# Performance work log

Hardware: AMD Instinct MI355X
Metric: run time of the kernel (lower is better)

Reference implementation:

```python
import jax, jax.numpy as jnp
import numpy as np

H = 64          # hidden_size
NG = 5000       # num_genes
B = 32          # num_graphs
N = B * NG      # total nodes
E = 1_600_000   # total edges


def setup_inputs() -> dict:
    key = jax.random.key(0)
    ks = jax.random.split(key, 32)
    def nrm(k, shape, s=0.05):
        return jax.random.normal(k, shape, jnp.float32) * s
    return {
        "x": jax.random.normal(ks[0], (N, 2), jnp.float32),
        "edge_index": jax.random.randint(ks[1], (2, E), 0, N),
        # pert_w: Linear(1, H); gene_basal_w: Linear(1, H)
        "pert_w_W": nrm(ks[2], (H, 1)), "pert_w_b": nrm(ks[3], (H,)),
        "basal_W": nrm(ks[4], (H, 1)), "basal_b": nrm(ks[5], (H,)),
        # gene embedding table (max_norm=True -> rows renormed to norm<=1)
        "emb_table": nrm(ks[6], (NG, H), 0.5),
        # emb_trans: Linear(2H, H)
        "emb_trans_W": nrm(ks[7], (H, 2 * H)), "emb_trans_b": nrm(ks[8], (H,)),
        # pert_base_trans_w: Linear(2H, H)  (gene_pert_agg == 'concat+w')
        "pbt_W": nrm(ks[9], (H, 2 * H)), "pbt_b": nrm(ks[10], (H,)),
        # two GCNConv(H, H) layers
        "gcn1_W": nrm(ks[11], (H, H)), "gcn1_b": nrm(ks[12], (H,)),
        "gcn2_W": nrm(ks[13], (H, H)), "gcn2_b": nrm(ks[14], (H,)),
        # recovery_w: MLP([H, 2H, H, 1]) with BN on first two hidden layers
        "rec_W1": nrm(ks[15], (2 * H, H)), "rec_b1": nrm(ks[16], (2 * H,)),
        "rec_g1": jnp.ones((2 * H,), jnp.float32), "rec_be1": jnp.zeros((2 * H,), jnp.float32),
        "rec_W2": nrm(ks[17], (H, 2 * H)), "rec_b2": nrm(ks[18], (H,)),
        "rec_g2": jnp.ones((H,), jnp.float32), "rec_be2": jnp.zeros((H,), jnp.float32),
        "rec_W3": nrm(ks[19], (1, H)), "rec_b3": nrm(ks[20], (1,)),
    }


def _gcn_conv(h, src, dst, norm, W, b, n_nodes):
    # PyG GCNConv: x' = scatter_add(norm * (x W^T)[src] -> dst) + b, self-loops included in src/dst
    m = h @ W.T                                   # [N, H]
    out = jax.ops.segment_sum(m[src] * norm[:, None], dst, num_segments=n_nodes)
    return out + b


def _batchnorm(z, g, b, eps=1e-5):
    mu = z.mean(0)
    var = z.var(0)
    return (z - mu) * jax.lax.rsqrt(var + eps) * g + b


def reference(x, edge_index, pert_w_W, pert_w_b, basal_W, basal_b, emb_table,
              emb_trans_W, emb_trans_b, pbt_W, pbt_b, gcn1_W, gcn1_b,
              gcn2_W, gcn2_b, rec_W1, rec_b1, rec_g1, rec_be1,
              rec_W2, rec_b2, rec_g2, rec_be2, rec_W3, rec_b3):
    n_nodes = x.shape[0]
    ng = emb_table.shape[0]
    nb = n_nodes // ng

    # GCN normalization with self-loops (computed once, shared by both layers)
    loop = jnp.arange(n_nodes)
    src = jnp.concatenate([edge_index[0], loop])
    dst = jnp.concatenate([edge_index[1], loop])
    deg = jax.ops.segment_sum(jnp.ones_like(src, jnp.float32), dst, num_segments=n_nodes)
    dinv = jnp.where(deg > 0, jax.lax.rsqrt(jnp.maximum(deg, 1.0)), 0.0)
    norm = dinv[src] * dinv[dst]

    pert_emb = x[:, 1:2] @ pert_w_W.T + pert_w_b          # [N, H]
    base = x[:, 0:1] @ basal_W.T + basal_b                # [N, H]

    # nn.Embedding(max_norm=True): renorm rows to max L2 norm of 1
    nrm = jnp.linalg.norm(emb_table, axis=1, keepdims=True)
    emb_n = emb_table * jnp.minimum(1.0, 1.0 / jnp.maximum(nrm, 1e-7))
    emb = jnp.tile(emb_n, (nb, 1))                        # arange(NG).repeat(B) lookup
    base_emb = jnp.concatenate([emb, base], axis=1) @ emb_trans_W.T + emb_trans_b

    def pbt(p, b_):
        return jnp.concatenate([p, b_], axis=1) @ pbt_W.T + pbt_b

    h = pbt(pert_emb, base_emb)
    h = pbt(jax.nn.relu(_gcn_conv(h, src, dst, norm, gcn1_W, gcn1_b, n_nodes)), base_emb)
    h = pbt(jax.nn.relu(_gcn_conv(h, src, dst, norm, gcn2_W, gcn2_b, n_nodes)), base_emb)

    # recovery_w: Linear -> BN -> ReLU -> Linear -> BN -> ReLU -> Linear
    z = jax.nn.relu(_batchnorm(h @ rec_W1.T + rec_b1, rec_g1, rec_be1))
    z = jax.nn.relu(_batchnorm(z @ rec_W2.T + rec_b2, rec_g2, rec_be2))
    out = z @ rec_W3.T + rec_b3                           # [N, 1]
    return out.reshape(nb, ng)
```

## Files before the change

### kernel.cpp

```cpp
#include <hip/hip_runtime.h>


#define GS_GRID 2048
#define GS_BLK  256

enum { A1_=0, A0_=64, C1_=128, C0_=192, D1_=256, D0_=320,
       S1_=384, Q1_=512, SC1_=640, SH1_=768,
       S2_=896, Q2_=960, SC2_=1024, SH2_=1088,
       GD1_=1152, GA1_=1216, G00_=1280, CST_FLOATS=2048 };

__device__ __forceinline__ float wave_sum64(float v) {
#pragma unroll
  for (int o = 32; o; o >>= 1) v += __shfl_xor(v, o, 64);
  return v;
}

__device__ __forceinline__ int rfl(int v) { return __builtin_amdgcn_readfirstlane(v); }

__device__ __forceinline__ float rlane(float v, int k) {
  return __int_as_float(__builtin_amdgcn_readlane(__float_as_int(v), k));
}


__global__ __launch_bounds__(256) void hist_k(const int* __restrict__ ei,
                                              int* __restrict__ hist, int E) {
  __shared__ int h[256];
  const int t = threadIdx.x;
  h[t] = 0;
  __syncthreads();
  const int per = (E + gridDim.x - 1) / gridDim.x;
  const int beg = blockIdx.x * per, end = min(E, beg + per);
  for (int i = beg + t; i < end; i += 256)
    atomicAdd(&h[ei[E + i] >> 10], 1);
  __syncthreads();
  hist[blockIdx.x * 256 + t] = h[t];
}

__global__ void bscan_k(int* __restrict__ hist, int* __restrict__ bucketBase,
                        int* __restrict__ rowptrN, int E, int nblk) {
  const int t = threadIdx.x;
  int run = 0;
  for (int b = 0; b < nblk; ++b) {
    int v = hist[b * 256 + t];
    hist[b * 256 + t] = run;
    run += v;
  }
  __shared__ int sc[256];
  sc[t] = run; __syncthreads();
  for (int o = 1; o < 256; o <<= 1) {
    int x = sc[t]; if (t >= o) x += sc[t - o];
    __syncthreads(); sc[t] = x; __syncthreads();
  }
  bucketBase[t] = sc[t] - run;
  if (t == 255) { bucketBase[256] = sc[t]; rowptrN[0] = E; }
}

__global__ __launch_bounds__(256) void bucket_k(const int* __restrict__ ei,
                                                const int* __restrict__ hist,
                                                const int* __restrict__ bucketBase,
                                                int2* __restrict__ eb, int E) {
  __shared__ int cur[256];
  const int t = threadIdx.x;
  cur[t] = hist[blockIdx.x * 256 + t] + bucketBase[t];
  __syncthreads();
  const int per = (E + gridDim.x - 1) / gridDim.x;
  const int beg = blockIdx.x * per, end = min(E, beg + per);
  for (int i = beg + t; i < end; i += 256) {
    int s = ei[i], d = ei[E + i];
    int pos = atomicAdd(&cur[d >> 10], 1);
    eb[pos] = make_int2(s, d);
  }
}

__global__ __launch_bounds__(256) void csr_k(const int2* __restrict__ eb,
                                             const int* __restrict__ bucketBase,
                                             int* __restrict__ rowptr, float* __restrict__ dinv,
                                             int* __restrict__ col, int N) {
  __shared__ int cnt[1024];
  __shared__ int base[1024];
  __shared__ int red[256];
  const int t = threadIdx.x;
  const int k = blockIdx.x;
  const int nodeBeg = k << 10;
  const int segBeg = bucketBase[k], segEnd = bucketBase[k + 1];
#pragma unroll
  for (int j = t; j < 1024; j += 256) cnt[j] = 0;
  __syncthreads();
  for (int i = segBeg + t; i < segEnd; i += 256)
    atomicAdd(&cnt[eb[i].y & 1023], 1);
  __syncthreads();
  int c0 = cnt[4 * t], c1 = cnt[4 * t + 1], c2 = cnt[4 * t + 2], c3 = cnt[4 * t + 3];
  int ts = c0 + c1 + c2 + c3;
  red[t] = ts; __syncthreads();
  for (int o = 1; o < 256; o <<= 1) {
    int x = red[t]; if (t >= o) x += red[t - o];
    __syncthreads(); red[t] = x; __syncthreads();
  }
  int off = red[t] - ts;
  base[4 * t] = off;
  base[4 * t + 1] = off + c0;
  base[4 * t + 2] = off + c0 + c1;
  base[4 * t + 3] = off + c0 + c1 + c2;
#pragma unroll
  for (int u = 0; u < 4; ++u) {
    int j = 4 * t + u;
    int node = nodeBeg + j;
    if (node < N) {
      rowptr[node] = segBeg + base[j];
      dinv[node] = rsqrtf((float)(cnt[j] + 1));
    }
  }
  __syncthreads();
  cnt[4 * t] = base[4 * t]; cnt[4 * t + 1] = base[4 * t + 1];
  cnt[4 * t + 2] = base[4 * t + 2]; cnt[4 * t + 3] = base[4 * t + 3];
  __syncthreads();
  for (int i = segBeg + t; i < segEnd; i += 256) {
    int2 e = eb[i];
    int pos = atomicAdd(&cnt[e.y & 1023], 1);
    col[segBeg + pos] = e.x;
  }
}

__global__ void consts1_k(const float* __restrict__ pbtW, const float* __restrict__ pertW,
                          const float* __restrict__ pertB, const float* __restrict__ etW,
                          const float* __restrict__ basW, const float* __restrict__ basB,
                          const float* __restrict__ etB, float* __restrict__ cst) {
  int h = threadIdx.x;
  float a1 = 0, a0 = 0, c1 = 0, c0 = 0;
  for (int k = 0; k < 64; ++k) {
    float wp = pbtW[h * 128 + k];
    a1 = fmaf(wp, pertW[k], a1);
    a0 = fmaf(wp, pertB[k], a0);
    float we = etW[h * 128 + 64 + k];
    c1 = fmaf(we, basW[k], c1);
    c0 = fmaf(we, basB[k], c0);
  }
  cst[A1_ + h] = a1; cst[A0_ + h] = a0; cst[C1_ + h] = c1; cst[C0_ + h] = c0 + etB[h];
}

__global__ void consts2_k(const float* __restrict__ pbtW, const float* __restrict__ pbtB,
                          float* __restrict__ cst) {
  int h = threadIdx.x;
  float d1 = 0, d0 = 0;
  for (int k = 0; k < 64; ++k) {
    float w = pbtW[h * 128 + 64 + k];
    d1 = fmaf(w, cst[C1_ + k], d1);
    d0 = fmaf(w, cst[C0_ + k], d0);
  }
  cst[D1_ + h] = d1; cst[D0_ + h] = d0 + pbtB[h];
}

__global__ void consts3_k(const float* __restrict__ g1W, float* __restrict__ cst) {
  int h = threadIdx.x;
  float gd1 = 0, ga1 = 0, g00 = 0;
  for (int k = 0; k < 64; ++k) {
    float w = g1W[h * 64 + k];
    gd1 = fmaf(w, cst[D1_ + k], gd1);
    ga1 = fmaf(w, cst[A1_ + k], ga1);
    g00 = fmaf(w, cst[D0_ + k] + cst[A0_ + k], g00);
  }
  cst[GD1_ + h] = gd1; cst[GA1_ + h] = ga1; cst[G00_ + h] = g00;
}

template <bool NORM>
__global__ __launch_bounds__(256) void geneT_k(const float* __restrict__ in,
                                               const float* __restrict__ W, int ldw,
                                               float* __restrict__ out, int NG) {
  const int lane = threadIdx.x & 63;
  const int wid = blockIdx.x * 4 + (threadIdx.x >> 6);
  const int nw = gridDim.x * 4;
  float w[64];
#pragma unroll
  for (int j = 0; j < 16; ++j) {
    float4 v = *reinterpret_cast<const float4*>(W + lane * ldw + 4 * j);
    w[4 * j] = v.x; w[4 * j + 1] = v.y; w[4 * j + 2] = v.z; w[4 * j + 3] = v.w;
  }
  for (int g = wid; g < NG; g += nw) {
    float e = in[g * 64 + lane];
    if (NORM) {
      float sq = wave_sum64(e * e);
      float nrm = sqrtf(sq);
      float s = nrm > 1.f ? 1.f / nrm : 1.f;
      e *= s;
    }
    float acc = 0.f;
#pragma unroll
    for (int k = 0; k < 64; ++k) acc = fmaf(w[k], rlane(e, k), acc);
    out[g * 64 + lane] = acc;
  }
}

__global__ __launch_bounds__(256) void h0m1_k(const float* __restrict__ x,
                                              const float* __restrict__ embT2,
                                              const float* __restrict__ embTm1,
                                              const float* __restrict__ dinv,
                                              const float* __restrict__ cst,
                                              float* __restrict__ pb2, float* __restrict__ m1,
                                              int N, int NG) {
  int total = N * 16;
  for (int idx = blockIdx.x * blockDim.x + threadIdx.x; idx < total;
       idx += gridDim.x * blockDim.x) {
    int n = idx >> 4, q = idx & 15;
    int g = n % NG;
    float x0 = x[2 * n], x1 = x[2 * n + 1], dn = dinv[n];
    float4 e2 = *reinterpret_cast<const float4*>(embT2 + g * 64 + q * 4);
    float4 em = *reinterpret_cast<const float4*>(embTm1 + g * 64 + q * 4);
    float4 d1 = *reinterpret_cast<const float4*>(cst + D1_ + q * 4);
    float4 d0 = *reinterpret_cast<const float4*>(cst + D0_ + q * 4);
    float4 gd1 = *reinterpret_cast<const float4*>(cst + GD1_ + q * 4);
    float4 ga1 = *reinterpret_cast<const float4*>(cst + GA1_ + q * 4);
    float4 g00 = *reinterpret_cast<const float4*>(cst + G00_ + q * 4);
    float4 pv, mv;
    pv.x = fmaf(x0, d1.x, e2.x + d0.x); pv.y = fmaf(x0, d1.y, e2.y + d0.y);
    pv.z = fmaf(x0, d1.z, e2.z + d0.z); pv.w = fmaf(x0, d1.w, e2.w + d0.w);
    mv.x = dn * (fmaf(x0, gd1.x, fmaf(x1, ga1.x, em.x + g00.x)));
    mv.y = dn * (fmaf(x0, gd1.y, fmaf(x1, ga1.y, em.y + g00.y)));
    mv.z = dn * (fmaf(x0, gd1.z, fmaf(x1, ga1.z, em.z + g00.z)));
    mv.w = dn * (fmaf(x0, gd1.w, fmaf(x1, ga1.w, em.w + g00.w)));
    reinterpret_cast<float4*>(pb2)[idx] = pv;
    reinterpret_cast<float4*>(m1)[idx] = mv;
  }
}

#define XS_STRIDE 130
#define WS_STRIDE 68
#define OS_STRIDE 68
#define OS_WORDS  (128 * OS_STRIDE)
#define WS_WORDS  (64 * WS_STRIDE)
#define LDS_WORDS (OS_WORDS + WS_WORDS + 128)

template <int LDIN, bool BN, bool MUL_D, bool STATS>
__global__ __launch_bounds__(256, 4) void gemmt_k(const float* __restrict__ in, int inOff,
                                                  const float* __restrict__ W, int ldw,
                                                  const float* __restrict__ bias,
                                                  const float* __restrict__ bnsc,
                                                  const float* __restrict__ bnsh,
                                                  const float* __restrict__ addv,
                                                  const float* __restrict__ dinv,
                                                  float* __restrict__ out, int ldout,
                                                  float* __restrict__ sums,
                                                  float* __restrict__ sqs, int N) {
  __shared__ float lds[LDS_WORDS];
  float* Xs = lds;
  float* Ws = lds + OS_WORDS;
  float* sred = lds + OS_WORDS + WS_WORDS;
  const int t = threadIdx.x;
  const int base = blockIdx.x << 7;
  if (STATS && t < 128) sred[t] = 0.f;

#pragma unroll
  for (int c = 0; c < 16; ++c) {
    int lin = c * 256 + t;
    int cw = lin >> 6, kw = lin & 63;
    Ws[kw * WS_STRIDE + cw] = W[cw * ldw + kw];
  }
#pragma unroll
  for (int c = 0; c < 8; ++c) {
    int lin = c * 256 + t;
    int nl = lin >> 4, k4 = lin & 15;
    int row = base + nl; if (row >= N) row = N - 1;
    float4 v = *reinterpret_cast<const float4*>(in + (size_t)row * LDIN + inOff + 4 * k4);
    if (BN) {
      float4 sc = *reinterpret_cast<const float4*>(bnsc + 4 * k4);
      float4 sh = *reinterpret_cast<const float4*>(bnsh + 4 * k4);
      v.x = fmaxf(fmaf(v.x, sc.x, sh.x), 0.f);
      v.y = fmaxf(fmaf(v.y, sc.y, sh.y), 0.f);
      v.z = fmaxf(fmaf(v.z, sc.z, sh.z), 0.f);
      v.w = fmaxf(fmaf(v.w, sc.w, sh.w), 0.f);
    }
    Xs[(4 * k4 + 0) * XS_STRIDE + nl] = v.x;
    Xs[(4 * k4 + 1) * XS_STRIDE + nl] = v.y;
    Xs[(4 * k4 + 2) * XS_STRIDE + nl] = v.z;
    Xs[(4 * k4 + 3) * XS_STRIDE + nl] = v.w;
  }
  __syncthreads();

  const int ng = t & 31;
  const int c0 = (t >> 5) * 8;
  float acc[8][4];
#pragma unroll
  for (int i = 0; i < 8; ++i)
#pragma unroll
    for (int j = 0; j < 4; ++j) acc[i][j] = 0.f;
#pragma unroll 4
  for (int k = 0; k < 64; ++k) {
    float4 wa = *reinterpret_cast<const float4*>(Ws + k * WS_STRIDE + c0);
    float4 wb = *reinterpret_cast<const float4*>(Ws + k * WS_STRIDE + c0 + 4);
    float2 xa = *reinterpret_cast<const float2*>(Xs + k * XS_STRIDE + 2 * ng);
    float2 xb = *reinterpret_cast<const float2*>(Xs + k * XS_STRIDE + 2 * ng + 64);
    const float w8[8] = {wa.x, wa.y, wa.z, wa.w, wb.x, wb.y, wb.z, wb.w};
    const float x4[4] = {xa.x, xa.y, xb.x, xb.y};
#pragma unroll
    for (int ci = 0; ci < 8; ++ci)
#pragma unroll
      for (int xi = 0; xi < 4; ++xi)
        acc[ci][xi] = fmaf(w8[ci], x4[xi], acc[ci][xi]);
  }
  __syncthreads();

  const int nd[4] = {2 * ng, 2 * ng + 1, 2 * ng + 64, 2 * ng + 65};
#pragma unroll
  for (int ci = 0; ci < 8; ++ci) {
    Xs[nd[0] * OS_STRIDE + c0 + ci] = acc[ci][0];
    Xs[nd[1] * OS_STRIDE + c0 + ci] = acc[ci][1];
    Xs[nd[2] * OS_STRIDE + c0 + ci] = acc[ci][2];
    Xs[nd[3] * OS_STRIDE + c0 + ci] = acc[ci][3];
  }
  __syncthreads();

  const int q = t & 15;
  float4 bb = make_float4(0.f, 0.f, 0.f, 0.f);
  if (bias) bb = *reinterpret_cast<const float4*>(bias + 4 * q);
  float4 s4 = make_float4(0.f, 0.f, 0.f, 0.f);
  float4 q4 = make_float4(0.f, 0.f, 0.f, 0.f);
#pragma unroll
  for (int c = 0; c < 8; ++c) {
    int nl = c * 16 + (t >> 4);
    int n = base + nl;
    if (n < N) {
      float4 o = *reinterpret_cast<const float4*>(Xs + nl * OS_STRIDE + 4 * q);
      if (MUL_D) {
        float dv = dinv[n];
        o.x *= dv; o.y *= dv; o.z *= dv; o.w *= dv;
      }
      o.x += bb.x; o.y += bb.y; o.z += bb.z; o.w += bb.w;
      if (addv) {
        float4 av = *reinterpret_cast<const float4*>(addv + (size_t)n * 64 + 4 * q);
        o.x += av.x; o.y += av.y; o.z += av.z; o.w += av.w;
      }
      *reinterpret_cast<float4*>(out + (size_t)n * ldout + 4 * q) = o;
      if (STATS) {
        s4.x += o.x; s4.y += o.y; s4.z += o.z; s4.w += o.w;
        q4.x += o.x * o.x; q4.y += o.y * o.y; q4.z += o.z * o.z; q4.w += o.w * o.w;
      }
    }
  }
  if (STATS) {
    atomicAdd(&sred[4 * q + 0], s4.x);
    atomicAdd(&sred[4 * q + 1], s4.y);
    atomicAdd(&sred[4 * q + 2], s4.z);
    atomicAdd(&sred[4 * q + 3], s4.w);
    atomicAdd(&sred[64 + 4 * q + 0], q4.x);
    atomicAdd(&sred[64 + 4 * q + 1], q4.y);
    atomicAdd(&sred[64 + 4 * q + 2], q4.z);
    atomicAdd(&sred[64 + 4 * q + 3], q4.w);
    __syncthreads();
    if (t < 64) {
      atomicAdd(&sums[t], sred[t]);
      atomicAdd(&sqs[t], sred[64 + t]);
    }
  }
}

__global__ __launch_bounds__(256) void gather_k(const float* __restrict__ m,
                                                const int* __restrict__ rowptr,
                                                const int* __restrict__ col,
                                                const float* __restrict__ dinv,
                                                const float* __restrict__ bias,
                                                float* __restrict__ out, int N) {
  const int lane = threadIdx.x & 63;
  const int wid = blockIdx.x * 4 + (threadIdx.x >> 6);
  const int nw = gridDim.x * 4;
  const float b = bias[lane];
  for (int n = wid; n < N; n += nw) {
    const int nn = rfl(n);
    const float dn = dinv[nn];
    float acc = m[(size_t)nn * 64 + lane];
    float acc2 = 0.f;
    const int beg = rfl(rowptr[nn]), end = rfl(rowptr[nn + 1]);
    for (int base = beg; base < end; base += 64) {
      const int rem = end - base;
      const int kk = rem < 64 ? rem : 64;
      int cv = (lane < kk) ? col[base + lane] : 0;
      int k = 0;
      for (; k + 3 < kk; k += 4) {
        int i0 = __shfl(cv, k, 64), i1 = __shfl(cv, k + 1, 64);
        int i2 = __shfl(cv, k + 2, 64), i3 = __shfl(cv, k + 3, 64);
        float v0 = m[(size_t)i0 * 64 + lane];
        float v1 = m[(size_t)i1 * 64 + lane];
        float v2 = m[(size_t)i2 * 64 + lane];
        float v3 = m[(size_t)i3 * 64 + lane];
        acc += v0 + v2; acc2 += v1 + v3;
      }
      for (; k < kk; ++k) acc += m[(size_t)__shfl(cv, k, 64) * 64 + lane];
    }
    out[(size_t)nn * 64 + lane] = fmaxf(fmaf(dn, acc + acc2, b), 0.f);
  }
}

__global__ void bnparam_k(const float* __restrict__ sums, const float* __restrict__ sqs,
                          const float* __restrict__ g, const float* __restrict__ be,
                          float* __restrict__ scale, float* __restrict__ shift, int C,
                          float invN) {
  int t = threadIdx.x;
  if (t < C) {
    float mu = sums[t] * invN;
    float var = fmaxf(sqs[t] * invN - mu * mu, 0.f);
    float sc = g[t] * rsqrtf(var + 1e-5f);
    scale[t] = sc;
    shift[t] = be[t] - mu * sc;
  }
}

__global__ __launch_bounds__(256) void rec3_k(const float* __restrict__ z2,
                                              const float* __restrict__ scale,
                                              const float* __restrict__ shift,
                                              const float* __restrict__ W3,
                                              const float* __restrict__ b3,
                                              float* __restrict__ out, int N) {
  const int lane = threadIdx.x & 63;
  const int wid = blockIdx.x * 4 + (threadIdx.x >> 6);
  const int nw = gridDim.x * 4;
  const float sc = scale[lane], sh = shift[lane], w = W3[lane], b = b3[0];
  for (int n = wid; n < N; n += nw) {
    float v = z2[(size_t)n * 64 + lane];
    v = fmaxf(fmaf(v, sc, sh), 0.f) * w;
    v = wave_sum64(v);
    if (lane == 0) out[n] = v + b;
  }
}

extern "C" void kernel_launch(void* const* d_in, const int* in_sizes, int n_in,
                              void* d_out, int out_size, void* d_ws, size_t ws_size,
                              hipStream_t stream) {
  const float* x     = (const float*)d_in[0];
  const int*   ei    = (const int*)d_in[1];
  const float* pertW = (const float*)d_in[2];
  const float* pertB = (const float*)d_in[3];
  const float* basW  = (const float*)d_in[4];
  const float* basB  = (const float*)d_in[5];
  const float* embTb = (const float*)d_in[6];
  const float* etW   = (const float*)d_in[7];
  const float* etB   = (const float*)d_in[8];
  const float* pbtW  = (const float*)d_in[9];
  const float* pbtB  = (const float*)d_in[10];
  const float* g1W   = (const float*)d_in[11];
  const float* g1B   = (const float*)d_in[12];
  const float* g2W   = (const float*)d_in[13];
  const float* g2B   = (const float*)d_in[14];
  const float* rW1   = (const float*)d_in[15];
  const float* rb1   = (const float*)d_in[16];
  const float* rg1   = (const float*)d_in[17];
  const float* rbe1  = (const float*)d_in[18];
  const float* rW2   = (const float*)d_in[19];
  const float* rb2   = (const float*)d_in[20];
  const float* rg2   = (const float*)d_in[21];
  const float* rbe2  = (const float*)d_in[22];
  const float* rW3   = (const float*)d_in[23];
  const float* rb3   = (const float*)d_in[24];
  float* outp = (float*)d_out;

  const int N  = in_sizes[0] / 2;
  const int E  = in_sizes[1] / 2;
  const int NG = in_sizes[6] / 64;
  const int NB = (N + 1023) >> 10;
  const int NT = (N + 127) >> 7;

  char* p = (char*)d_ws;
  float* cst   = (float*)p; p += CST_FLOATS * 4;
  int*   hist  = (int*)p;   p += 256 * 256 * 4;
  int*   bb    = (int*)p;   p += 1024;
  int*   rowptr= (int*)p;   p += (size_t)(N + 64) * 4;
  float* dinv  = (float*)p; p += (size_t)N * 4;
  int*   col   = (int*)p;   p += (size_t)E * 4;
  float* embT  = (float*)p; p += (size_t)NG * 64 * 4;
  float* embT2 = (float*)p; p += (size_t)NG * 64 * 4;
  float* pb2   = (float*)p; p += (size_t)N * 64 * 4;
  float* hb    = (float*)p; p += (size_t)N * 64 * 4;
  float* tmp1  = (float*)p; p += (size_t)N * 64 * 4;
  float* tmp2  = (float*)p; p += (size_t)N * 64 * 4;
  float* Z   = tmp1;
  float* z2  = pb2;
  float* prt = hb;
  float* embTm1 = embT;
  int2*  eb = (int2*)tmp2;

  dim3 blk(GS_BLK), grid(GS_GRID);

  hipMemsetAsync(cst, 0, CST_FLOATS * 4, stream);

  hist_k<<<256, 256, 0, stream>>>(ei, hist, E);
  bscan_k<<<1, 256, 0, stream>>>(hist, bb, rowptr + N, E, 256);
  bucket_k<<<256, 256, 0, stream>>>(ei, hist, bb, eb, E);
  csr_k<<<NB, 256, 0, stream>>>(eb, bb, rowptr, dinv, col, N);

  consts1_k<<<1, 64, 0, stream>>>(pbtW, pertW, pertB, etW, basW, basB, etB, cst);
  consts2_k<<<1, 64, 0, stream>>>(pbtW, pbtB, cst);
  consts3_k<<<1, 64, 0, stream>>>(g1W, cst);
  geneT_k<true><<<256, 256, 0, stream>>>(embTb, etW, 128, embT, NG);
  geneT_k<false><<<256, 256, 0, stream>>>(embT, pbtW + 64, 128, embT2, NG);
  geneT_k<false><<<256, 256, 0, stream>>>(embT2, g1W, 64, embTm1, NG);
  h0m1_k<<<grid, blk, 0, stream>>>(x, embT2, embTm1, dinv, cst, pb2, tmp1, N, NG);

  gather_k<<<grid, blk, 0, stream>>>(tmp1, rowptr, col, dinv, g1B, tmp2, N);
  gemmt_k<64, false, false, false><<<NT, blk, 0, stream>>>(
      tmp2, 0, pbtW, 128, nullptr, nullptr, nullptr, pb2, nullptr, hb, 64,
      nullptr, nullptr, N);
  gemmt_k<64, false, true, false><<<NT, blk, 0, stream>>>(
      hb, 0, g2W, 64, nullptr, nullptr, nullptr, nullptr, dinv, tmp1, 64,
      nullptr, nullptr, N);
  gather_k<<<grid, blk, 0, stream>>>(tmp1, rowptr, col, dinv, g2B, tmp2, N);
  gemmt_k<64, false, false, false><<<NT, blk, 0, stream>>>(
      tmp2, 0, pbtW, 128, nullptr, nullptr, nullptr, pb2, nullptr, hb, 64,
      nullptr, nullptr, N);

  gemmt_k<64, false, false, true><<<NT, blk, 0, stream>>>(
      hb, 0, rW1, 64, rb1, nullptr, nullptr, nullptr, nullptr, Z, 128,
      cst + S1_, cst + Q1_, N);
  gemmt_k<64, false, false, true><<<NT, blk, 0, stream>>>(
      hb, 0, rW1 + 64 * 64, 64, rb1 + 64, nullptr, nullptr, nullptr, nullptr, Z + 64, 128,
      cst + S1_ + 64, cst + Q1_ + 64, N);
  bnparam_k<<<1, 128, 0, stream>>>(cst + S1_, cst + Q1_, rg1, rbe1,
                                   cst + SC1_, cst + SH1_, 128, 1.0f / (float)N);
  gemmt_k<128, true, false, false><<<NT, blk, 0, stream>>>(
      Z, 0, rW2, 128, nullptr, cst + SC1_, cst + SH1_, nullptr, nullptr, prt, 64,
      nullptr, nullptr, N);
  gemmt_k<128, true, false, true><<<NT, blk, 0, stream>>>(
      Z, 64, rW2 + 64, 128, rb2, cst + SC1_ + 64, cst + SH1_ + 64, prt, nullptr, z2, 64,
      cst + S2_, cst + Q2_, N);
  bnparam_k<<<1, 64, 0, stream>>>(cst + S2_, cst + Q2_, rg2, rbe2,
                                  cst + SC2_, cst + SH2_, 64, 1.0f / (float)N);
  rec3_k<<<grid, blk, 0, stream>>>(z2, cst + SC2_, cst + SH2_, rW3, rb3, outp, N);
}
```

Baseline: 580.2 us.

## Fold pbt linear into following GEMMs and fuse rec2 halves into one kernel

Precomputes composed weights g2W·pbtW and rW1·pbtW plus per-gene and per-feature constant tables, so the pbt projection after each GCN layer is merged algebraically into the next GEMM. This removes the pb2 buffer and the per-node addv reads, along with two full N×64 GEMM passes. The second recovery layer now runs both K-halves in one kernel with a shared accumulator, so the partial-output round trip is gone. Costs are a few extra tiny setup kernels, gene-table lookups in the GEMM epilogue, and a different floating-point summation order.

```diff
diff --git a/kernel.cpp b/kernel.cpp
--- a/kernel.cpp
+++ b/kernel.cpp
@@ -7,7 +7,8 @@
 enum { A1_=0, A0_=64, C1_=128, C0_=192, D1_=256, D0_=320,
        S1_=384, Q1_=512, SC1_=640, SH1_=768,
        S2_=896, Q2_=960, SC2_=1024, SH2_=1088,
-       GD1_=1152, GA1_=1216, G00_=1280, CST_FLOATS=2048 };
+       GD1_=1152, GA1_=1216, G00_=1280,
+       GD2_=1344, G02_=1408, RD1_=1472, RD0_=1600, CST_FLOATS=2048 };
 
 __device__ __forceinline__ float wave_sum64(float v) {
 #pragma unroll
@@ -162,6 +163,47 @@
   cst[GD1_ + h] = gd1; cst[GA1_ + h] = ga1; cst[G00_ + h] = g00;
 }
 
+__global__ void consts5_k(const float* __restrict__ g2W, float* __restrict__ cst) {
+  int h = threadIdx.x;
+  float a = 0, b = 0;
+  for (int k = 0; k < 64; ++k) {
+    float w = g2W[h * 64 + k];
+    a = fmaf(w, cst[D1_ + k], a);
+    b = fmaf(w, cst[D0_ + k], b);
+  }
+  cst[GD2_ + h] = a; cst[G02_ + h] = b;
+}
+
+__global__ void consts6_k(const float* __restrict__ rW1, const float* __restrict__ rb1,
+                          float* __restrict__ cst) {
+  int c = threadIdx.x;
+  float a = 0, b = 0;
+  for (int k = 0; k < 64; ++k) {
+    float w = rW1[c * 64 + k];
+    a = fmaf(w, cst[D1_ + k], a);
+    b = fmaf(w, cst[D0_ + k], b);
+  }
+  cst[RD1_ + c] = a; cst[RD0_ + c] = b + rb1[c];
+}
+
+__global__ void constsW_k(const float* __restrict__ g2W, const float* __restrict__ rW1,
+                          const float* __restrict__ pbtW,
+                          float* __restrict__ Wf, float* __restrict__ Wr) {
+  const int t = threadIdx.x;
+  for (int e = t; e < 4096; e += 256) {
+    int c = e >> 6, j = e & 63;
+    float s = 0.f;
+    for (int h = 0; h < 64; ++h) s = fmaf(g2W[c * 64 + h], pbtW[h * 128 + j], s);
+    Wf[e] = s;
+  }
+  for (int e = t; e < 8192; e += 256) {
+    int c = e >> 6, j = e & 63;
+    float s = 0.f;
+    for (int h = 0; h < 64; ++h) s = fmaf(rW1[c * 64 + h], pbtW[h * 128 + j], s);
+    Wr[e] = s;
+  }
+}
+
 template <bool NORM>
 __global__ __launch_bounds__(256) void geneT_k(const float* __restrict__ in,
                                                const float* __restrict__ W, int ldw,
@@ -190,34 +232,26 @@
   }
 }
 
-__global__ __launch_bounds__(256) void h0m1_k(const float* __restrict__ x,
-                                              const float* __restrict__ embT2,
-                                              const float* __restrict__ embTm1,
-                                              const float* __restrict__ dinv,
-                                              const float* __restrict__ cst,
-                                              float* __restrict__ pb2, float* __restrict__ m1,
-                                              int N, int NG) {
+__global__ __launch_bounds__(256) void m1_k(const float* __restrict__ x,
+                                            const float* __restrict__ embTm1,
+                                            const float* __restrict__ dinv,
+                                            const float* __restrict__ cst,
+                                            float* __restrict__ m1, int N, int NG) {
   int total = N * 16;
   for (int idx = blockIdx.x * blockDim.x + threadIdx.x; idx < total;
        idx += gridDim.x * blockDim.x) {
     int n = idx >> 4, q = idx & 15;
     int g = n % NG;
     float x0 = x[2 * n], x1 = x[2 * n + 1], dn = dinv[n];
-    float4 e2 = *reinterpret_cast<const float4*>(embT2 + g * 64 + q * 4);
     float4 em = *reinterpret_cast<const float4*>(embTm1 + g * 64 + q * 4);
-    float4 d1 = *reinterpret_cast<const float4*>(cst + D1_ + q * 4);
-    float4 d0 = *reinterpret_cast<const float4*>(cst + D0_ + q * 4);
     float4 gd1 = *reinterpret_cast<const float4*>(cst + GD1_ + q * 4);
     float4 ga1 = *reinterpret_cast<const float4*>(cst + GA1_ + q * 4);
     float4 g00 = *reinterpret_cast<const float4*>(cst + G00_ + q * 4);
-    float4 pv, mv;
-    pv.x = fmaf(x0, d1.x, e2.x + d0.x); pv.y = fmaf(x0, d1.y, e2.y + d0.y);
-    pv.z = fmaf(x0, d1.z, e2.z + d0.z); pv.w = fmaf(x0, d1.w, e2.w + d0.w);
+    float4 mv;
     mv.x = dn * (fmaf(x0, gd1.x, fmaf(x1, ga1.x, em.x + g00.x)));
     mv.y = dn * (fmaf(x0, gd1.y, fmaf(x1, ga1.y, em.y + g00.y)));
     mv.z = dn * (fmaf(x0, gd1.z, fmaf(x1, ga1.z, em.z + g00.z)));
     mv.w = dn * (fmaf(x0, gd1.w, fmaf(x1, ga1.w, em.w + g00.w)));
-    reinterpret_cast<float4*>(pb2)[idx] = pv;
     reinterpret_cast<float4*>(m1)[idx] = mv;
   }
 }
@@ -229,17 +263,17 @@
 #define WS_WORDS  (64 * WS_STRIDE)
 #define LDS_WORDS (OS_WORDS + WS_WORDS + 128)
 
-template <int LDIN, bool BN, bool MUL_D, bool STATS>
-__global__ __launch_bounds__(256, 4) void gemmt_k(const float* __restrict__ in, int inOff,
-                                                  const float* __restrict__ W, int ldw,
-                                                  const float* __restrict__ bias,
-                                                  const float* __restrict__ bnsc,
-                                                  const float* __restrict__ bnsh,
-                                                  const float* __restrict__ addv,
-                                                  const float* __restrict__ dinv,
-                                                  float* __restrict__ out, int ldout,
-                                                  float* __restrict__ sums,
-                                                  float* __restrict__ sqs, int N) {
+template <bool MUL_D, bool STATS>
+__global__ __launch_bounds__(256, 4) void gemmt_gv_k(
+    const float* __restrict__ in,
+    const float* __restrict__ W,
+    const float* __restrict__ tbl,
+    const float* __restrict__ cA,
+    const float* __restrict__ cB,
+    const float* __restrict__ x,
+    const float* __restrict__ dinv,
+    float* __restrict__ out, int ldout,
+    float* __restrict__ sums, float* __restrict__ sqs, int N, int NG) {
   __shared__ float lds[LDS_WORDS];
   float* Xs = lds;
   float* Ws = lds + OS_WORDS;
@@ -252,22 +286,14 @@
   for (int c = 0; c < 16; ++c) {
     int lin = c * 256 + t;
     int cw = lin >> 6, kw = lin & 63;
-    Ws[kw * WS_STRIDE + cw] = W[cw * ldw + kw];
+    Ws[kw * WS_STRIDE + cw] = W[cw * 64 + kw];
   }
 #pragma unroll
   for (int c = 0; c < 8; ++c) {
     int lin = c * 256 + t;
     int nl = lin >> 4, k4 = lin & 15;
     int row = base + nl; if (row >= N) row = N - 1;
-    float4 v = *reinterpret_cast<const float4*>(in + (size_t)row * LDIN + inOff + 4 * k4);
-    if (BN) {
-      float4 sc = *reinterpret_cast<const float4*>(bnsc + 4 * k4);
-      float4 sh = *reinterpret_cast<const float4*>(bnsh + 4 * k4);
-      v.x = fmaxf(fmaf(v.x, sc.x, sh.x), 0.f);
-      v.y = fmaxf(fmaf(v.y, sc.y, sh.y), 0.f);
-      v.z = fmaxf(fmaf(v.z, sc.z, sh.z), 0.f);
-      v.w = fmaxf(fmaf(v.w, sc.w, sh.w), 0.f);
-    }
+    float4 v = *reinterpret_cast<const float4*>(in + (size_t)row * 64 + 4 * k4);
     Xs[(4 * k4 + 0) * XS_STRIDE + nl] = v.x;
     Xs[(4 * k4 + 1) * XS_STRIDE + nl] = v.y;
     Xs[(4 * k4 + 2) * XS_STRIDE + nl] = v.z;
@@ -309,8 +335,8 @@
   __syncthreads();
 
   const int q = t & 15;
-  float4 bb = make_float4(0.f, 0.f, 0.f, 0.f);
-  if (bias) bb = *reinterpret_cast<const float4*>(bias + 4 * q);
+  const float4 a4 = *reinterpret_cast<const float4*>(cA + 4 * q);
+  const float4 b4 = *reinterpret_cast<const float4*>(cB + 4 * q);
   float4 s4 = make_float4(0.f, 0.f, 0.f, 0.f);
   float4 q4 = make_float4(0.f, 0.f, 0.f, 0.f);
 #pragma unroll
@@ -319,14 +345,16 @@
     int n = base + nl;
     if (n < N) {
       float4 o = *reinterpret_cast<const float4*>(Xs + nl * OS_STRIDE + 4 * q);
+      int g = n % NG;
+      float4 tg = *reinterpret_cast<const float4*>(tbl + (size_t)g * 64 + 4 * q);
+      float x0 = x[2 * n];
+      o.x += fmaf(x0, a4.x, tg.x + b4.x);
+      o.y += fmaf(x0, a4.y, tg.y + b4.y);
+      o.z += fmaf(x0, a4.z, tg.z + b4.z);
+      o.w += fmaf(x0, a4.w, tg.w + b4.w);
       if (MUL_D) {
         float dv = dinv[n];
         o.x *= dv; o.y *= dv; o.z *= dv; o.w *= dv;
-      }
-      o.x += bb.x; o.y += bb.y; o.z += bb.z; o.w += bb.w;
-      if (addv) {
-        float4 av = *reinterpret_cast<const float4*>(addv + (size_t)n * 64 + 4 * q);
-        o.x += av.x; o.y += av.y; o.z += av.z; o.w += av.w;
       }
       *reinterpret_cast<float4*>(out + (size_t)n * ldout + 4 * q) = o;
       if (STATS) {
@@ -349,6 +377,114 @@
       atomicAdd(&sums[t], sred[t]);
       atomicAdd(&sqs[t], sred[64 + t]);
     }
+  }
+}
+
+__global__ __launch_bounds__(256, 4) void gemmt_rec2_k(
+    const float* __restrict__ Z,
+    const float* __restrict__ W,
+    const float* __restrict__ b,
+    const float* __restrict__ bnsc, const float* __restrict__ bnsh,
+    float* __restrict__ out,
+    float* __restrict__ sums, float* __restrict__ sqs, int N) {
+  __shared__ float lds[LDS_WORDS];
+  float* Xs = lds;
+  float* Ws = lds + OS_WORDS;
+  float* sred = lds + OS_WORDS + WS_WORDS;
+  const int t = threadIdx.x;
+  const int base = blockIdx.x << 7;
+  if (t < 128) sred[t] = 0.f;
+
+  const int ng = t & 31;
+  const int c0 = (t >> 5) * 8;
+  float acc[8][4];
+#pragma unroll
+  for (int i = 0; i < 8; ++i)
+#pragma unroll
+    for (int j = 0; j < 4; ++j) acc[i][j] = 0.f;
+
+  for (int half = 0; half < 2; ++half) {
+    if (half) __syncthreads();
+    const int ko = half * 64;
+#pragma unroll
+    for (int c = 0; c < 16; ++c) {
+      int lin = c * 256 + t;
+      int cw = lin >> 6, kw = lin & 63;
+      Ws[kw * WS_STRIDE + cw] = W[cw * 128 + ko + kw];
+    }
+#pragma unroll
+    for (int c = 0; c < 8; ++c) {
+      int lin = c * 256 + t;
+      int nl = lin >> 4, k4 = lin & 15;
+      int row = base + nl; if (row >= N) row = N - 1;
+      float4 v = *reinterpret_cast<const float4*>(Z + (size_t)row * 128 + ko + 4 * k4);
+      float4 sc = *reinterpret_cast<const float4*>(bnsc + ko + 4 * k4);
+      float4 sh = *reinterpret_cast<const float4*>(bnsh + ko + 4 * k4);
+      v.x = fmaxf(fmaf(v.x, sc.x, sh.x), 0.f);
+      v.y = fmaxf(fmaf(v.y, sc.y, sh.y), 0.f);
+      v.z = fmaxf(fmaf(v.z, sc.z, sh.z), 0.f);
+      v.w = fmaxf(fmaf(v.w, sc.w, sh.w), 0.f);
+      Xs[(4 * k4 + 0) * XS_STRIDE + nl] = v.x;
+      Xs[(4 * k4 + 1) * XS_STRIDE + nl] = v.y;
+      Xs[(4 * k4 + 2) * XS_STRIDE + nl] = v.z;
+      Xs[(4 * k4 + 3) * XS_STRIDE + nl] = v.w;
+    }
+    __syncthreads();
+#pragma unroll 4
+    for (int k = 0; k < 64; ++k) {
+      float4 wa = *reinterpret_cast<const float4*>(Ws + k * WS_STRIDE + c0);
+      float4 wb = *reinterpret_cast<const float4*>(Ws + k * WS_STRIDE + c0 + 4);
+      float2 xa = *reinterpret_cast<const float2*>(Xs + k * XS_STRIDE + 2 * ng);
+      float2 xb = *reinterpret_cast<const float2*>(Xs + k * XS_STRIDE + 2 * ng + 64);
+      const float w8[8] = {wa.x, wa.y, wa.z, wa.w, wb.x, wb.y, wb.z, wb.w};
+      const float x4[4] = {xa.x, xa.y, xb.x, xb.y};
+#pragma unroll
+      for (int ci = 0; ci < 8; ++ci)
+#pragma unroll
+        for (int xi = 0; xi < 4; ++xi)
+          acc[ci][xi] = fmaf(w8[ci], x4[xi], acc[ci][xi]);
+    }
+  }
+  __syncthreads();
+
+  const int nd[4] = {2 * ng, 2 * ng + 1, 2 * ng + 64, 2 * ng + 65};
+#pragma unroll
+  for (int ci = 0; ci < 8; ++ci) {
+    Xs[nd[0] * OS_STRIDE + c0 + ci] = acc[ci][0];
+    Xs[nd[1] * OS_STRIDE + c0 + ci] = acc[ci][1];
+    Xs[nd[2] * OS_STRIDE + c0 + ci] = acc[ci][2];
+    Xs[nd[3] * OS_STRIDE + c0 + ci] = acc[ci][3];
+  }
+  __syncthreads();
+
+  const int q = t & 15;
+  const float4 bb = *reinterpret_cast<const float4*>(b + 4 * q);
+  float4 s4 = make_float4(0.f, 0.f, 0.f, 0.f);
+  float4 q4 = make_float4(0.f, 0.f, 0.f, 0.f);
+#pragma unroll
+  for (int c = 0; c < 8; ++c) {
+    int nl = c * 16 + (t >> 4);
+    int n = base + nl;
+    if (n < N) {
+      float4 o = *reinterpret_cast<const float4*>(Xs + nl * OS_STRIDE + 4 * q);
+      o.x += bb.x; o.y += bb.y; o.z += bb.z; o.w += bb.w;
+      *reinterpret_cast<float4*>(out + (size_t)n * 64 + 4 * q) = o;
+      s4.x += o.x; s4.y += o.y; s4.z += o.z; s4.w += o.w;
+      q4.x += o.x * o.x; q4.y += o.y * o.y; q4.z += o.z * o.z; q4.w += o.w * o.w;
+    }
+  }
+  atomicAdd(&sred[4 * q + 0], s4.x);
+  atomicAdd(&sred[4 * q + 1], s4.y);
+  atomicAdd(&sred[4 * q + 2], s4.z);
+  atomicAdd(&sred[4 * q + 3], s4.w);
+  atomicAdd(&sred[64 + 4 * q + 0], q4.x);
+  atomicAdd(&sred[64 + 4 * q + 1], q4.y);
+  atomicAdd(&sred[64 + 4 * q + 2], q4.z);
+  atomicAdd(&sred[64 + 4 * q + 3], q4.w);
+  __syncthreads();
+  if (t < 64) {
+    atomicAdd(&sums[t], sred[t]);
+    atomicAdd(&sqs[t], sred[64 + t]);
   }
 }
 
@@ -457,21 +593,25 @@
   const int NT = (N + 127) >> 7;
 
   char* p = (char*)d_ws;
-  float* cst   = (float*)p; p += CST_FLOATS * 4;
-  int*   hist  = (int*)p;   p += 256 * 256 * 4;
-  int*   bb    = (int*)p;   p += 1024;
-  int*   rowptr= (int*)p;   p += (size_t)(N + 64) * 4;
-  float* dinv  = (float*)p; p += (size_t)N * 4;
-  int*   col   = (int*)p;   p += (size_t)E * 4;
-  float* embT  = (float*)p; p += (size_t)NG * 64 * 4;
-  float* embT2 = (float*)p; p += (size_t)NG * 64 * 4;
-  float* pb2   = (float*)p; p += (size_t)N * 64 * 4;
-  float* hb    = (float*)p; p += (size_t)N * 64 * 4;
-  float* tmp1  = (float*)p; p += (size_t)N * 64 * 4;
-  float* tmp2  = (float*)p; p += (size_t)N * 64 * 4;
-  float* Z   = tmp1;
-  float* z2  = pb2;
-  float* prt = hb;
+  float* cst    = (float*)p; p += CST_FLOATS * 4;
+  int*   hist   = (int*)p;   p += 256 * 256 * 4;
+  int*   bb     = (int*)p;   p += 1024;
+  int*   rowptr = (int*)p;   p += (size_t)(N + 64) * 4;
+  float* dinv   = (float*)p; p += (size_t)N * 4;
+  int*   col    = (int*)p;   p += (size_t)E * 4;
+  float* Wf     = (float*)p; p += 4096 * 4;
+  float* Wr     = (float*)p; p += 8192 * 4;
+  float* embT   = (float*)p; p += (size_t)NG * 64 * 4;
+  float* embT2  = (float*)p; p += (size_t)NG * 64 * 4;
+  float* embT2g2= (float*)p; p += (size_t)NG * 64 * 4;
+  float* embT2rA= (float*)p; p += (size_t)NG * 64 * 4;
+  float* embT2rB= (float*)p; p += (size_t)NG * 64 * 4;
+  float* z2buf  = (float*)p; p += (size_t)N * 64 * 4;
+  float* hb     = (float*)p; p += (size_t)N * 64 * 4;
+  float* tmp1   = (float*)p; p += (size_t)N * 64 * 4;
+  float* tmp2   = (float*)p; p += (size_t)N * 64 * 4;
+  float* Z = hb;
+  float* z2 = z2buf;
   float* embTm1 = embT;
   int2*  eb = (int2*)tmp2;
 
@@ -487,37 +627,33 @@
   consts1_k<<<1, 64, 0, stream>>>(pbtW, pertW, pertB, etW, basW, basB, etB, cst);
   consts2_k<<<1, 64, 0, stream>>>(pbtW, pbtB, cst);
   consts3_k<<<1, 64, 0, stream>>>(g1W, cst);
+  consts5_k<<<1, 64, 0, stream>>>(g2W, cst);
+  consts6_k<<<1, 128, 0, stream>>>(rW1, rb1, cst);
+  constsW_k<<<1, 256, 0, stream>>>(g2W, rW1, pbtW, Wf, Wr);
   geneT_k<true><<<256, 256, 0, stream>>>(embTb, etW, 128, embT, NG);
   geneT_k<false><<<256, 256, 0, stream>>>(embT, pbtW + 64, 128, embT2, NG);
   geneT_k<false><<<256, 256, 0, stream>>>(embT2, g1W, 64, embTm1, NG);
-  h0m1_k<<<grid, blk, 0, stream>>>(x, embT2, embTm1, dinv, cst, pb2, tmp1, N, NG);
+  geneT_k<false><<<256, 256, 0, stream>>>(embT2, g2W, 64, embT2g2, NG);
+  geneT_k<false><<<256, 256, 0, stream>>>(embT2, rW1, 64, embT2rA, NG);
+  geneT_k<false><<<256, 256, 0, stream>>>(embT2, rW1 + 64 * 64, 64, embT2rB, NG);
+  m1_k<<<grid, blk, 0, stream>>>(x, embTm1, dinv, cst, tmp1, N, NG);
 
   gather_k<<<grid, blk, 0, stream>>>(tmp1, rowptr, col, dinv, g1B, tmp2, N);
-  gemmt_k<64, false, false, false><<<NT, blk, 0, stream>>>(
-      tmp2, 0, pbtW, 128, nullptr, nullptr, nullptr, pb2, nullptr, hb, 64,
-      nullptr, nullptr, N);
-  gemmt_k<64, false, true, false><<<NT, blk, 0, stream>>>(
-      hb, 0, g2W, 64, nullptr, nullptr, nullptr, nullptr, dinv, tmp1, 64,
-      nullptr, nullptr, N);
+  gemmt_gv_k<true, false><<<NT, blk, 0, stream>>>(
+      tmp2, Wf, embT2g2, cst + GD2_, cst + G02_, x, dinv, tmp1, 64,
+      nullptr, nullptr, N, NG);
   gather_k<<<grid, blk, 0, stream>>>(tmp1, rowptr, col, dinv, g2B, tmp2, N);
-  gemmt_k<64, false, false, false><<<NT, blk, 0, stream>>>(
-      tmp2, 0, pbtW, 128, nullptr, nullptr, nullptr, pb2, nullptr, hb, 64,
-      nullptr, nullptr, N);
-
-  gemmt_k<64, false, false, true><<<NT, blk, 0, stream>>>(
-      hb, 0, rW1, 64, rb1, nullptr, nullptr, nullptr, nullptr, Z, 128,
-      cst + S1_, cst + Q1_, N);
-  gemmt_k<64, false, false, true><<<NT, blk, 0, stream>>>(
-      hb, 0, rW1 + 64 * 64, 64, rb1 + 64, nullptr, nullptr, nullptr, nullptr, Z + 64, 128,
-      cst + S1_ + 64, cst + Q1_ + 64, N);
+
+  gemmt_gv_k<false, true><<<NT, blk, 0, stream>>>(
+      tmp2, Wr, embT2rA, cst + RD1_, cst + RD0_, x, nullptr, Z, 128,
+      cst + S1_, cst + Q1_, N, NG);
+  gemmt_gv_k<false, true><<<NT, blk, 0, stream>>>(
+      tmp2, Wr + 64 * 64, embT2rB, cst + RD1_ + 64, cst + RD0_ + 64, x, nullptr,
+      Z + 64, 128, cst + S1_ + 64, cst + Q1_ + 64, N, NG);
   bnparam_k<<<1, 128, 0, stream>>>(cst + S1_, cst + Q1_, rg1, rbe1,
                                    cst + SC1_, cst + SH1_, 128, 1.0f / (float)N);
-  gemmt_k<128, true, false, false><<<NT, blk, 0, stream>>>(
-      Z, 0, rW2, 128, nullptr, cst + SC1_, cst + SH1_, nullptr, nullptr, prt, 64,
-      nullptr, nullptr, N);
-  gemmt_k<128, true, false, true><<<NT, blk, 0, stream>>>(
-      Z, 64, rW2 + 64, 128, rb2, cst + SC1_ + 64, cst + SH1_ + 64, prt, nullptr, z2, 64,
-      cst + S2_, cst + Q2_, N);
+  gemmt_rec2_k<<<NT, blk, 0, stream>>>(Z, rW2, rb2, cst + SC1_, cst + SH1_,
+                                       z2, cst + S2_, cst + Q2_, N);
   bnparam_k<<<1, 64, 0, stream>>>(cst + S2_, cst + Q2_, rg2, rbe2,
                                   cst + SC2_, cst + SH2_, 64, 1.0f / (float)N);
   rec3_k<<<grid, blk, 0, stream>>>(z2, cst + SC2_, cst + SH2_, rW3, rb3, outp, N);
```

New measurement: 569.2 us. Within noise of the previous version (-1.9%).
